# Performance work log

Measured on AMD Instinct MI355X. Metric: run time of the kernel, lower is better.

## Reference

```python
import jax, jax.numpy as jnp
import numpy as np

N, C, H, W = 4, 256, 60, 60
CIMG = 5  # rgb/ir channels after add_position (3 + x + y)
K = 8
ITERS = 2


def setup_inputs() -> dict:
    key = jax.random.key(0)
    ks = jax.random.split(key, 12)
    inp = {
        "cnn_encoder_output": jax.random.normal(ks[0], (N, C, H, W), jnp.float32),
        "rgb": jax.random.normal(ks[1], (N, CIMG, H, W), jnp.float32),
        "ir": jax.random.normal(ks[2], (N, CIMG, H, W), jnp.float32),
        # g-MLP (mlp_num_layers=1): Linear(2C -> C), torch weight layout [out, in]
        "W_g_rgb": jax.random.normal(ks[3], (C, 2 * C), jnp.float32) * 0.02,
        "b_g_rgb": jnp.zeros((C,), jnp.float32),
        "W_g_ir": jax.random.normal(ks[4], (C, 2 * C), jnp.float32) * 0.02,
        "b_g_ir": jnp.zeros((C,), jnp.float32),
        # SE block: Linear(2C -> C//16) -> ReLU -> Linear(C//16 -> C) -> Sigmoid
        "W_se1": jax.random.normal(ks[5], (C // 16, 2 * C), jnp.float32) * 0.02,
        "b_se1": jnp.zeros((C // 16,), jnp.float32),
        "W_se2": jax.random.normal(ks[6], (C, C // 16), jnp.float32) * 0.02,
        "b_se2": jnp.zeros((C,), jnp.float32),
        "gamma": jnp.ones((1,), jnp.float32),
        "gnn_iterations": ITERS,
        "k": K,
    }
    return inp


def _knn_indices(x, k):
    # x: [N, HW, D] -> indices of k nearest neighbours [N, HW, k]
    r = jnp.einsum("nid,njd->nij", x, x)          # gram matrix
    sq = jnp.einsum("nid,nid->ni", x, x)          # squared norms
    d2 = sq[:, :, None] + sq[:, None, :] - 2.0 * r
    d = jnp.sqrt(jnp.maximum(d2, 0.0))
    d = jax.lax.stop_gradient(d)
    _, idx = jax.lax.top_k(-d, k)                  # smallest distances
    return idx


def _gather(h, idx):
    # h: [N, HW, C], idx: [N, HW, K] -> [N, HW, K, C]
    return jax.vmap(lambda hn, i: hn[i])(h, idx)


def reference(cnn_encoder_output, rgb, ir, W_g_rgb, b_g_rgb, W_g_ir, b_g_ir,
              W_se1, b_se1, W_se2, b_se2, gamma, gnn_iterations, k):
    n, c, hh, ww = cnn_encoder_output.shape
    hw = hh * ww
    rgb_f = rgb.reshape(n, rgb.shape[1], hw).transpose(0, 2, 1)  # [N, HW, 5]
    ir_f = ir.reshape(n, ir.shape[1], hw).transpose(0, 2, 1)
    knn_rgb = _knn_indices(rgb_f, k)  # [N, HW, K]
    knn_ir = _knn_indices(ir_f, k)

    h = cnn_encoder_output.transpose(0, 2, 3, 1).reshape(n, hw, c)  # [N, HW, C]

    for _ in range(gnn_iterations):
        rgb_nb = _gather(h, knn_rgb)  # [N, HW, K, C]
        ir_nb = _gather(h, knn_ir)
        rgb_feat = jnp.concatenate([rgb_nb, rgb_nb - ir_nb], axis=-1)  # [N,HW,K,2C]
        ir_feat = jnp.concatenate([ir_nb, ir_nb - rgb_nb], axis=-1)
        m_rgb = jnp.max(jax.nn.relu(jnp.einsum("nhkf,cf->nhkc", rgb_feat, W_g_rgb) + b_g_rgb), axis=2)
        m_ir = jnp.max(jax.nn.relu(jnp.einsum("nhkf,cf->nhkc", ir_feat, W_g_ir) + b_g_ir), axis=2)
        cc = jnp.concatenate([m_rgb, m_ir], axis=-1).mean(axis=1, keepdims=True)  # [N,1,2C]
        se = jax.nn.sigmoid(jax.nn.relu(cc @ W_se1.T + b_se1) @ W_se2.T + b_se2)  # [N,1,C]
        h = se * h

    h = h.reshape(n, hh, ww, c).transpose(0, 3, 1, 2)
    return jax.nn.relu(gamma * h + cnn_encoder_output)
```

## Files before the change

### kernel.cpp

```cpp
#include <hip/hip_runtime.h>
#include <hip/hip_bf16.h>

#define NB 4
#define CH 256
#define HWT 3600
#define KNN 8
#define ITERS 2
#define POSB 16
#define MPAD 3712

#define SSEG 16
#define SEGJ 225

typedef __attribute__((ext_vector_type(8))) __bf16 bf16x8;
typedef __attribute__((ext_vector_type(4))) float f32x4;

__device__ inline float med3f(float a, float b, float c) {
    return __builtin_amdgcn_fmed3f(a, b, c);
}

__global__ void knn_prep(const float* __restrict__ rgb, const float* __restrict__ ir,
                         float* __restrict__ xpack) {
    int t = blockIdx.x * blockDim.x + threadIdx.x;
    if (t >= 2 * NB * HWT) return;
    int nm = t / HWT, j = t - nm * HWT;
    int mod = nm / NB, n = nm - mod * NB;
    const float* x = (mod == 0 ? rgb : ir) + (size_t)n * 5 * HWT;
    float v[5], q = 0.f;
#pragma unroll
    for (int d = 0; d < 5; ++d) { v[d] = x[d * HWT + j]; q = fmaf(v[d], v[d], q); }
    float* o = xpack + (size_t)t * 8;
#pragma unroll
    for (int d = 0; d < 5; ++d) o[d] = v[d];
    o[5] = q; o[6] = 0.f; o[7] = 0.f;
}

__global__ __launch_bounds__(256) void knn_main(const float* __restrict__ xpack,
                                                unsigned* __restrict__ partial) {
    int seg = blockIdx.x, rb = blockIdx.y, nm = blockIdx.z;
    int t = threadIdx.x;
    const float* xp = xpack + (size_t)nm * HWT * 8;
    __shared__ float4 xs[SEGJ * 2];
    const float4* src = ((const float4*)xp) + seg * (SEGJ * 2);
    xs[t] = src[t];
    if (t + 256 < SEGJ * 2) xs[t + 256] = src[t + 256];
    __syncthreads();

    int row = rb * SEGJ + t;
    bool active = (t < SEGJ);
    int rr = active ? row : 0;
    float4 a0 = ((const float4*)xp)[rr * 2];
    float4 b0 = ((const float4*)xp)[rr * 2 + 1];
    float xi0 = a0.x, xi1 = a0.y, xi2 = a0.z, xi3 = a0.w, xi4 = b0.x;
    float qi1 = b0.y + 1.0f;

    const float BIG = __uint_as_float(0x7F000000u);
    float best[8];
#pragma unroll
    for (int i = 0; i < 8; ++i) best[i] = BIG;

    const float2* xs2 = (const float2*)xs;
    unsigned jg0 = (unsigned)(seg * SEGJ);
#pragma unroll 5
    for (int jj = 0; jj < SEGJ; ++jj) {
        float4 a = xs[jj * 2];
        float2 b = xs2[jj * 4 + 2];
        float dot = a.x * xi0;
        dot = fmaf(a.y, xi1, dot);
        dot = fmaf(a.z, xi2, dot);
        dot = fmaf(a.w, xi3, dot);
        dot = fmaf(b.x, xi4, dot);
        float d2 = fmaf(-2.0f, dot, b.y + qi1);
        unsigned kb = (__float_as_uint(d2) & 0xFFFFF000u) | (jg0 + jj);
        float kf = __uint_as_float(kb);
        best[7] = med3f(best[6], best[7], kf);
        best[6] = med3f(best[5], best[6], kf);
        best[5] = med3f(best[4], best[5], kf);
        best[4] = med3f(best[3], best[4], kf);
        best[3] = med3f(best[2], best[3], kf);
        best[2] = med3f(best[1], best[2], kf);
        best[1] = med3f(best[0], best[1], kf);
        best[0] = fminf(best[0], kf);
    }
    if (active) {
        unsigned* o = partial + (((size_t)nm * SSEG + seg) * HWT + row) * 8;
        uint4 lo = { __float_as_uint(best[0]), __float_as_uint(best[1]),
                     __float_as_uint(best[2]), __float_as_uint(best[3]) };
        uint4 hi = { __float_as_uint(best[4]), __float_as_uint(best[5]),
                     __float_as_uint(best[6]), __float_as_uint(best[7]) };
        ((uint4*)o)[0] = lo;
        ((uint4*)o)[1] = hi;
    }
}

__global__ __launch_bounds__(256) void knn_merge(const unsigned* __restrict__ partial,
                                                 int* __restrict__ knn_rgb,
                                                 int* __restrict__ knn_ir) {
    int tid = blockIdx.x * blockDim.x + threadIdx.x;
    if (tid >= 2 * 2 * NB * HWT) return;
    int rid = tid >> 1, sub = tid & 1;
    int nm = rid / HWT, row = rid - nm * HWT;
    const float BIG = __uint_as_float(0x7F000000u);
    float best[8];
#pragma unroll
    for (int i = 0; i < 8; ++i) best[i] = BIG;
    for (int s = sub; s < SSEG; s += 2) {
        const unsigned* p = partial + (((size_t)nm * SSEG + s) * HWT + row) * 8;
#pragma unroll
        for (int w = 0; w < 2; ++w) {
            uint4 v = ((const uint4*)p)[w];
            unsigned vv[4] = { v.x, v.y, v.z, v.w };
#pragma unroll
            for (int e = 0; e < 4; ++e) {
                float kf = __uint_as_float(vv[e]);
                best[7] = med3f(best[6], best[7], kf);
                best[6] = med3f(best[5], best[6], kf);
                best[5] = med3f(best[4], best[5], kf);
                best[4] = med3f(best[3], best[4], kf);
                best[3] = med3f(best[2], best[3], kf);
                best[2] = med3f(best[1], best[2], kf);
                best[1] = med3f(best[0], best[1], kf);
                best[0] = fminf(best[0], kf);
            }
        }
    }
    float other[8];
#pragma unroll
    for (int i = 0; i < 8; ++i) other[i] = __shfl_xor(best[i], 1);
#pragma unroll
    for (int i = 0; i < 8; ++i) {
        float kf = other[i];
        best[7] = med3f(best[6], best[7], kf);
        best[6] = med3f(best[5], best[6], kf);
        best[5] = med3f(best[4], best[5], kf);
        best[4] = med3f(best[3], best[4], kf);
        best[3] = med3f(best[2], best[3], kf);
        best[2] = med3f(best[1], best[2], kf);
        best[1] = med3f(best[0], best[1], kf);
        best[0] = fminf(best[0], kf);
    }
    if (sub == 0) {
        int mod = nm / NB, n = nm - mod * NB;
        int* o = (mod == 0 ? knn_rgb : knn_ir) + ((size_t)n * HWT + row) * KNN;
#pragma unroll
        for (int i = 0; i < 8; ++i) o[i] = (int)(__float_as_uint(best[i]) & 0xFFFu);
    }
}

__global__ void init_kernel(const float* __restrict__ Wg_rgb, const float* __restrict__ Wg_ir,
                            float* __restrict__ Wcomb, float* __restrict__ g) {
    int t = blockIdx.x * blockDim.x + threadIdx.x;
    if (t < 1024 * 256) {
        int o = t >> 8, j = t & 255;
        float v;
        if (o < 256)      v = Wg_rgb[o * 512 + j] + Wg_rgb[o * 512 + 256 + j];
        else if (o < 512) v = Wg_rgb[(o - 256) * 512 + 256 + j];
        else if (o < 768) v = Wg_ir[(o - 512) * 512 + j] + Wg_ir[(o - 512) * 512 + 256 + j];
        else              v = Wg_ir[(o - 768) * 512 + 256 + j];
        Wcomb[t] = v;
    }
    if (t < NB * CH) g[t] = 1.0f;
}

__global__ __launch_bounds__(256) void scale_w(const float* __restrict__ Wcomb,
                                               const float* __restrict__ g,
                                               __hip_bfloat16* __restrict__ Wbf) {
    int n = blockIdx.y;
    int gid = blockIdx.x * 256 + threadIdx.x;
    int o = gid >> 5;
    int kb = (gid & 31) * 8;
    const float* w = Wcomb + o * 256 + kb;
    const float* gp = g + n * CH + kb;
    union { uint4 u; __hip_bfloat16 h[8]; } pk;
#pragma unroll
    for (int i = 0; i < 8; ++i) pk.h[i] = __float2bfloat16(w[i] * gp[i]);
    *(uint4*)(Wbf + ((size_t)n * 1024 + o) * CH + kb) = pk.u;
}

__global__ __launch_bounds__(256) void convert_a(const float* __restrict__ cnn,
                                                 __hip_bfloat16* __restrict__ Abf) {
    __shared__ float st[64][65];
    int n = blockIdx.z, k0 = blockIdx.y * 64, m0 = blockIdx.x * 64;
    int t = threadIdx.x;
    const float* src = cnn + (size_t)n * CH * HWT;
#pragma unroll
    for (int r = 0; r < 4; ++r) {
        int kl = r * 16 + (t >> 4);
        int ms = (t & 15) * 4;
        float4 v = {0.f, 0.f, 0.f, 0.f};
        if (m0 + ms < HWT) v = *(const float4*)(src + (size_t)(k0 + kl) * HWT + m0 + ms);
        st[ms + 0][kl] = v.x; st[ms + 1][kl] = v.y;
        st[ms + 2][kl] = v.z; st[ms + 3][kl] = v.w;
    }
    __syncthreads();
    int m = t >> 2, kg = (t & 3) * 16;
    union { uint4 u[2]; __hip_bfloat16 h[16]; } pk;
#pragma unroll
    for (int i = 0; i < 16; ++i) pk.h[i] = __float2bfloat16(st[m][kg + i]);
    __hip_bfloat16* dst = Abf + ((size_t)n * MPAD + m0 + m) * CH + k0 + kg;
    ((uint4*)dst)[0] = pk.u[0];
    ((uint4*)dst)[1] = pk.u[1];
}

__global__ __launch_bounds__(256) void gemm_mfma(const __hip_bfloat16* __restrict__ Abf,
                                                 const __hip_bfloat16* __restrict__ Wbf,
                                                 __hip_bfloat16* __restrict__ Yall) {
    __shared__ char smem[32768];
    char* sA = smem;
    char* sB = smem + 16384;
    int lid = blockIdx.x;
    int n = blockIdx.y;
    int w = (lid & 7) * 29 + (lid >> 3);
    int m0 = (w >> 3) * 128;
    int o0 = (w & 7) * 128;
    int t = threadIdx.x;
    int lane = t & 63, wid = t >> 6;
    int wm = wid >> 1, wo = wid & 1;

    const __hip_bfloat16* Ab = Abf + (size_t)n * MPAD * CH;
    const __hip_bfloat16* Wb = Wbf + (size_t)n * 1024 * CH;

    f32x4 acc[4][4] = {};

    int srow = t >> 3;
    int sslot = t & 7;
    int swz = (sslot ^ (srow & 7)) << 4;
    int fr = lane & 15;
    int kg = lane >> 4;
    int p = lane & 7;

    uint4 av[4], bv[4];
    auto load_tile = [&](int ks) {
#pragma unroll
        for (int r = 0; r < 4; ++r) {
            int row = srow + 32 * r;
            av[r] = *(const uint4*)(Ab + ((size_t)(m0 + row)) * CH + ks * 64 + sslot * 8);
            bv[r] = *(const uint4*)(Wb + ((size_t)(o0 + row)) * CH + ks * 64 + sslot * 8);
        }
    };
    load_tile(0);

    for (int ks = 0; ks < 4; ++ks) {
        __syncthreads();
#pragma unroll
        for (int r = 0; r < 4; ++r) {
            int row = srow + 32 * r;
            *(uint4*)(sA + row * 128 + swz) = av[r];
            *(uint4*)(sB + row * 128 + swz) = bv[r];
        }
        __syncthreads();
        if (ks < 3) load_tile(ks + 1);
#pragma unroll
        for (int kk = 0; kk < 2; ++kk) {
            bf16x8 hf[4], wf[4];
            int slot = kk * 4 + kg;
            int inrow = (slot ^ p) << 4;
#pragma unroll
            for (int f = 0; f < 4; ++f) {
                hf[f] = *(const bf16x8*)(sA + (wm * 64 + f * 16 + fr) * 128 + inrow);
                wf[f] = *(const bf16x8*)(sB + (wo * 64 + f * 16 + fr) * 128 + inrow);
            }
#pragma unroll
            for (int fa = 0; fa < 4; ++fa)
#pragma unroll
                for (int fb = 0; fb < 4; ++fb)
                    acc[fa][fb] = __builtin_amdgcn_mfma_f32_16x16x32_bf16(
                        wf[fa], hf[fb], acc[fa][fb], 0, 0, 0);
        }
    }

    __syncthreads();
#pragma unroll
    for (int fa = 0; fa < 4; ++fa)
#pragma unroll
        for (int fb = 0; fb < 4; ++fb) {
            int ml = wm * 64 + fb * 16 + fr;
            int ob = (wo * 64 + fa * 16 + kg * 4) * 2;
            f32x4 v = acc[fa][fb];
            union { ushort4 u; __hip_bfloat16 h[4]; } pk;
            pk.h[0] = __float2bfloat16(v.x);
            pk.h[1] = __float2bfloat16(v.y);
            pk.h[2] = __float2bfloat16(v.z);
            pk.h[3] = __float2bfloat16(v.w);
            int swzb = (ob & ~15) ^ ((ml & 15) << 4);
            *(ushort4*)(smem + ml * 256 + swzb + (ob & 15)) = pk.u;
        }
    __syncthreads();
    __hip_bfloat16* Y = Yall + (size_t)n * HWT * 1024;
    int colb = (t & 15) * 16;
#pragma unroll
    for (int i = 0; i < 8; ++i) {
        int row = i * 16 + (t >> 4);
        int grow = m0 + row;
        if (grow < HWT) {
            uint4 v = *(const uint4*)(smem + row * 256 + (colb ^ ((row & 15) << 4)));
            *(uint4*)((char*)Y + (size_t)grow * 2048 + o0 * 2 + colb) = v;
        }
    }
}

__global__ void zero_cc(float* __restrict__ ccsum) {
    int t = blockIdx.x * blockDim.x + threadIdx.x;
    if (t < NB * 512) ccsum[t] = 0.f;
}

__global__ __launch_bounds__(256) void gather_kernel(const __hip_bfloat16* __restrict__ Yall,
                                                     const int* __restrict__ knn_rgb,
                                                     const int* __restrict__ knn_ir,
                                                     const float* __restrict__ b_rgb,
                                                     const float* __restrict__ b_ir,
                                                     float* __restrict__ ccsum) {
    int lid = blockIdx.x;
    int xcd = lid & 7, sub = lid >> 3;
    int wg = (xcd < 4 ? xcd * 113 : 4 * 113 + (xcd - 4) * 112) + sub;
    int n = wg / 225;
    int hwbase = (wg - n * 225) * POSB;
    int t = threadIdx.x;
    int half = t >> 7;
    int cp = (t & 127) << 1;
    __shared__ int sidx[POSB][2][KNN];
    {
        int p = t >> 4, rem = t & 15;
        int hw = hwbase + p;
        int v;
        if (rem < 8) v = knn_rgb[((size_t)n * HWT + hw) * KNN + rem];
        else         v = knn_ir[((size_t)n * HWT + hw) * KNN + (rem - 8)];
        sidx[p][rem >> 3][rem & 7] = v;
    }
    __syncthreads();
    const float* bias = half ? b_ir : b_rgb;
    float b0 = bias[cp], b1 = bias[cp + 1];
    float acc0 = 0.f, acc1 = 0.f;
    const __hip_bfloat16* Y = Yall + (size_t)n * HWT * 1024;
    int offA = half * 512 + cp;
    int offB = half * 512 + 256 + cp;
    for (int p = 0; p < POSB; ++p) {
        float m0 = 0.f, m1 = 0.f;
#pragma unroll
        for (int k = 0; k < KNN; ++k) {
            int jA = sidx[p][half][k];
            int jB = sidx[p][half ^ 1][k];
            unsigned u1 = *(const unsigned*)(Y + (size_t)jA * 1024 + offA);
            unsigned u2 = *(const unsigned*)(Y + (size_t)jB * 1024 + offB);
            float a0 = __uint_as_float(u1 << 16);
            float a1 = __uint_as_float(u1 & 0xFFFF0000u);
            float c0 = __uint_as_float(u2 << 16);
            float c1 = __uint_as_float(u2 & 0xFFFF0000u);
            m0 = fmaxf(m0, a0 - c0 + b0);
            m1 = fmaxf(m1, a1 - c1 + b1);
        }
        acc0 += m0;
        acc1 += m1;
    }
    atomicAdd(&ccsum[n * 512 + half * 256 + cp], acc0);
    atomicAdd(&ccsum[n * 512 + half * 256 + cp + 1], acc1);
}

__global__ __launch_bounds__(256) void se_kernel(const float* __restrict__ ccsum,
                                                 const float* __restrict__ W1,
                                                 const float* __restrict__ b1,
                                                 const float* __restrict__ W2,
                                                 const float* __restrict__ b2,
                                                 float* __restrict__ g) {
    int n = blockIdx.x;
    int t = threadIdx.x;
    __shared__ float hid[16];
    __shared__ float cc[512];
    cc[t] = ccsum[n * 512 + t] * (1.0f / HWT);
    cc[256 + t] = ccsum[n * 512 + 256 + t] * (1.0f / HWT);
    __syncthreads();
    if (t < 16) {
        float s = b1[t];
        for (int j = 0; j < 512; ++j) s = fmaf(W1[t * 512 + j], cc[j], s);
        hid[t] = fmaxf(s, 0.f);
    }
    __syncthreads();
    float s = b2[t];
#pragma unroll
    for (int q = 0; q < 16; ++q) s = fmaf(W2[t * 16 + q], hid[q], s);
    float se = 1.0f / (1.0f + expf(-s));
    g[n * CH + t] *= se;
}

__global__ void final_kernel(const float* __restrict__ cnn, const float* __restrict__ g,
                             const float* __restrict__ gamma, float* __restrict__ out) {
    int t = blockIdx.x * blockDim.x + threadIdx.x;
    if (t >= NB * CH * HWT / 4) return;
    int nc = (t * 4) / HWT;
    float4 x = ((const float4*)cnn)[t];
    float s = gamma[0] * g[nc] + 1.0f;
    float4 o;
    o.x = fmaxf(s * x.x, 0.f);
    o.y = fmaxf(s * x.y, 0.f);
    o.z = fmaxf(s * x.z, 0.f);
    o.w = fmaxf(s * x.w, 0.f);
    ((float4*)out)[t] = o;
}

extern "C" void kernel_launch(void* const* d_in, const int* in_sizes, int n_in,
                              void* d_out, int out_size, void* d_ws, size_t ws_size,
                              hipStream_t stream) {
    const float* cnn    = (const float*)d_in[0];
    const float* rgb    = (const float*)d_in[1];
    const float* ir     = (const float*)d_in[2];
    const float* Wg_rgb = (const float*)d_in[3];
    const float* bg_rgb = (const float*)d_in[4];
    const float* Wg_ir  = (const float*)d_in[5];
    const float* bg_ir  = (const float*)d_in[6];
    const float* Wse1   = (const float*)d_in[7];
    const float* bse1   = (const float*)d_in[8];
    const float* Wse2   = (const float*)d_in[9];
    const float* bse2   = (const float*)d_in[10];
    const float* gamma  = (const float*)d_in[11];
    float* out = (float*)d_out;

    char* ws = (char*)d_ws;
    size_t off = 0;
    float* xpack = (float*)(ws + off); off += (size_t)2 * NB * HWT * 8 * 4;
    int* knn_rgb = (int*)(ws + off); off += (size_t)NB * HWT * KNN * 4;
    int* knn_ir  = (int*)(ws + off); off += (size_t)NB * HWT * KNN * 4;
    float* Wcomb = (float*)(ws + off); off += (size_t)1024 * 256 * 4;
    __hip_bfloat16* Wbf = (__hip_bfloat16*)(ws + off); off += (size_t)NB * 1024 * CH * 2;
    __hip_bfloat16* Abf = (__hip_bfloat16*)(ws + off); off += (size_t)NB * MPAD * CH * 2;
    __hip_bfloat16* Yall = (__hip_bfloat16*)(ws + off);
    unsigned* partial = (unsigned*)Yall;
    off += (size_t)NB * HWT * 1024 * 2;
    float* ccsum = (float*)(ws + off); off += (size_t)NB * 512 * 4;
    float* g     = (float*)(ws + off); off += (size_t)NB * CH * 4;

    knn_prep<<<(2 * NB * HWT + 255) / 256, 256, 0, stream>>>(rgb, ir, xpack);
    knn_main<<<dim3(SSEG, 16, 2 * NB), 256, 0, stream>>>(xpack, partial);
    knn_merge<<<(4 * NB * HWT + 255) / 256, 256, 0, stream>>>(partial, knn_rgb, knn_ir);
    init_kernel<<<1024, 256, 0, stream>>>(Wg_rgb, Wg_ir, Wcomb, g);
    convert_a<<<dim3(MPAD / 64, 4, NB), 256, 0, stream>>>(cnn, Abf);

    for (int it = 0; it < ITERS; ++it) {
        scale_w<<<dim3(128, NB), 256, 0, stream>>>(Wcomb, g, Wbf);
        gemm_mfma<<<dim3(232, NB), 256, 0, stream>>>(Abf, Wbf, Yall);
        zero_cc<<<8, 256, 0, stream>>>(ccsum);
        gather_kernel<<<NB * HWT / POSB, 256, 0, stream>>>(Yall, knn_rgb, knn_ir,
                                                           bg_rgb, bg_ir, ccsum);
        se_kernel<<<NB, 256, 0, stream>>>(ccsum, Wse1, bse1, Wse2, bse2, g);
    }
    final_kernel<<<(NB * CH * HWT / 4 + 255) / 256, 256, 0, stream>>>(cnn, g, gamma, out);
}
```

Measured before the change: 240.7 us.

## Fuse setup kernels and co-schedule first GEMM with KNN search

The independent setup kernels (A conversion, weight combining, KNN prep) are merged into one launch. The first-iteration GEMM runs in the same launch as the KNN distance search, with blocks interleaved so MFMA work and VALU work share the GPU. The first scale_w is skipped because g starts at one, and the zeroing of ccsum is folded into neighbouring kernels, which cuts the launch count. The KNN partial buffer now gets its own workspace instead of aliasing Yall, and segments change to 8 of 450 columns. This costs more workspace, and a single block now runs either GEMM or KNN, so the shared-memory and register budget is set by the heavier of the two.

```diff
diff --git a/kernel.cpp b/kernel.cpp
--- a/kernel.cpp
+++ b/kernel.cpp
@@ -5,12 +5,16 @@
 #define CH 256
 #define HWT 3600
 #define KNN 8
-#define ITERS 2
 #define POSB 16
 #define MPAD 3712
 
-#define SSEG 16
-#define SEGJ 225
+#define SSEGP 8
+#define SEGC 450
+#define ROWB 225
+
+#define GEMM_BLKS 928
+#define KNN_BLKS 1024
+#define B_BLKS 1952
 
 typedef __attribute__((ext_vector_type(8))) __bf16 bf16x8;
 typedef __attribute__((ext_vector_type(4))) float f32x4;
@@ -19,38 +23,128 @@
     return __builtin_amdgcn_fmed3f(a, b, c);
 }
 
-__global__ void knn_prep(const float* __restrict__ rgb, const float* __restrict__ ir,
-                         float* __restrict__ xpack) {
-    int t = blockIdx.x * blockDim.x + threadIdx.x;
-    if (t >= 2 * NB * HWT) return;
-    int nm = t / HWT, j = t - nm * HWT;
-    int mod = nm / NB, n = nm - mod * NB;
-    const float* x = (mod == 0 ? rgb : ir) + (size_t)n * 5 * HWT;
-    float v[5], q = 0.f;
-#pragma unroll
-    for (int d = 0; d < 5; ++d) { v[d] = x[d * HWT + j]; q = fmaf(v[d], v[d], q); }
-    float* o = xpack + (size_t)t * 8;
-#pragma unroll
-    for (int d = 0; d < 5; ++d) o[d] = v[d];
-    o[5] = q; o[6] = 0.f; o[7] = 0.f;
-}
-
-__global__ __launch_bounds__(256) void knn_main(const float* __restrict__ xpack,
-                                                unsigned* __restrict__ partial) {
-    int seg = blockIdx.x, rb = blockIdx.y, nm = blockIdx.z;
+
+__device__ __forceinline__ void gemm_body(int lid, int n,
+                                          const __hip_bfloat16* __restrict__ Abf,
+                                          const __hip_bfloat16* __restrict__ Wbf,
+                                          __hip_bfloat16* __restrict__ Yall,
+                                          char* smem) {
+    char* sA = smem;
+    char* sB = smem + 16384;
+    int w = (lid & 7) * 29 + (lid >> 3);
+    int m0 = (w >> 3) * 128;
+    int o0 = (w & 7) * 128;
+    int t = threadIdx.x;
+    int lane = t & 63, wid = t >> 6;
+    int wm = wid >> 1, wo = wid & 1;
+
+    const __hip_bfloat16* Ab = Abf + (size_t)n * MPAD * CH;
+    const __hip_bfloat16* Wb = Wbf + (size_t)n * 1024 * CH;
+
+    f32x4 acc[4][4] = {};
+
+    int srow = t >> 3;
+    int sslot = t & 7;
+    int swz = (sslot ^ (srow & 7)) << 4;
+    int fr = lane & 15;
+    int kg = lane >> 4;
+    int p = lane & 7;
+
+    uint4 av[4], bv[4];
+    auto load_tile = [&](int ks) {
+#pragma unroll
+        for (int r = 0; r < 4; ++r) {
+            int row = srow + 32 * r;
+            av[r] = *(const uint4*)(Ab + ((size_t)(m0 + row)) * CH + ks * 64 + sslot * 8);
+            bv[r] = *(const uint4*)(Wb + ((size_t)(o0 + row)) * CH + ks * 64 + sslot * 8);
+        }
+    };
+    load_tile(0);
+
+    for (int ks = 0; ks < 4; ++ks) {
+        __syncthreads();
+#pragma unroll
+        for (int r = 0; r < 4; ++r) {
+            int row = srow + 32 * r;
+            *(uint4*)(sA + row * 128 + swz) = av[r];
+            *(uint4*)(sB + row * 128 + swz) = bv[r];
+        }
+        __syncthreads();
+        if (ks < 3) load_tile(ks + 1);
+#pragma unroll
+        for (int kk = 0; kk < 2; ++kk) {
+            bf16x8 hf[4], wf[4];
+            int slot = kk * 4 + kg;
+            int inrow = (slot ^ p) << 4;
+#pragma unroll
+            for (int f = 0; f < 4; ++f) {
+                hf[f] = *(const bf16x8*)(sA + (wm * 64 + f * 16 + fr) * 128 + inrow);
+                wf[f] = *(const bf16x8*)(sB + (wo * 64 + f * 16 + fr) * 128 + inrow);
+            }
+#pragma unroll
+            for (int fa = 0; fa < 4; ++fa)
+#pragma unroll
+                for (int fb = 0; fb < 4; ++fb)
+                    acc[fa][fb] = __builtin_amdgcn_mfma_f32_16x16x32_bf16(
+                        wf[fa], hf[fb], acc[fa][fb], 0, 0, 0);
+        }
+    }
+
+    __syncthreads();
+#pragma unroll
+    for (int fa = 0; fa < 4; ++fa)
+#pragma unroll
+        for (int fb = 0; fb < 4; ++fb) {
+            int ml = wm * 64 + fb * 16 + fr;
+            int ob = (wo * 64 + fa * 16 + kg * 4) * 2;
+            f32x4 v = acc[fa][fb];
+            union { ushort4 u; __hip_bfloat16 h[4]; } pk;
+            pk.h[0] = __float2bfloat16(v.x);
+            pk.h[1] = __float2bfloat16(v.y);
+            pk.h[2] = __float2bfloat16(v.z);
+            pk.h[3] = __float2bfloat16(v.w);
+            int swzb = (ob & ~15) ^ ((ml & 15) << 4);
+            *(ushort4*)(smem + ml * 256 + swzb + (ob & 15)) = pk.u;
+        }
+    __syncthreads();
+    __hip_bfloat16* Y = Yall + (size_t)n * HWT * 1024;
+    int colb = (t & 15) * 16;
+#pragma unroll
+    for (int i = 0; i < 8; ++i) {
+        int row = i * 16 + (t >> 4);
+        int grow = m0 + row;
+        if (grow < HWT) {
+            uint4 v = *(const uint4*)(smem + row * 256 + (colb ^ ((row & 15) << 4)));
+            *(uint4*)((char*)Y + (size_t)grow * 2048 + o0 * 2 + colb) = v;
+        }
+    }
+}
+
+__device__ __forceinline__ void knn_body(int kid, const float* __restrict__ xpack,
+                                         unsigned* __restrict__ partial, char* smem) {
+    int seg = kid & 7;
+    int rb = (kid >> 3) & 15;
+    int nm = kid >> 7;
     int t = threadIdx.x;
     const float* xp = xpack + (size_t)nm * HWT * 8;
-    __shared__ float4 xs[SEGJ * 2];
-    const float4* src = ((const float4*)xp) + seg * (SEGJ * 2);
-    xs[t] = src[t];
-    if (t + 256 < SEGJ * 2) xs[t + 256] = src[t + 256];
-    __syncthreads();
-
-    int row = rb * SEGJ + t;
-    bool active = (t < SEGJ);
+    float4* xs4 = (float4*)smem;
+    float2* xs2 = (float2*)(smem + SEGC * 16);
+    int j0 = seg * SEGC;
+    for (int i = t; i < SEGC; i += 256) {
+        const float4* s = (const float4*)(xp + (size_t)(j0 + i) * 8);
+        float4 a = s[0];
+        float4 b = s[1];
+        xs4[i] = a;
+        float2 tmp; tmp.x = b.x; tmp.y = b.y;
+        xs2[i] = tmp;
+    }
+    __syncthreads();
+
+    int row = rb * ROWB + t;
+    bool active = (t < ROWB);
     int rr = active ? row : 0;
-    float4 a0 = ((const float4*)xp)[rr * 2];
-    float4 b0 = ((const float4*)xp)[rr * 2 + 1];
+    float4 a0 = ((const float4*)xp)[(size_t)rr * 2];
+    float4 b0 = ((const float4*)xp)[(size_t)rr * 2 + 1];
     float xi0 = a0.x, xi1 = a0.y, xi2 = a0.z, xi3 = a0.w, xi4 = b0.x;
     float qi1 = b0.y + 1.0f;
 
@@ -59,12 +153,11 @@
 #pragma unroll
     for (int i = 0; i < 8; ++i) best[i] = BIG;
 
-    const float2* xs2 = (const float2*)xs;
-    unsigned jg0 = (unsigned)(seg * SEGJ);
+    unsigned jg0 = (unsigned)j0;
 #pragma unroll 5
-    for (int jj = 0; jj < SEGJ; ++jj) {
-        float4 a = xs[jj * 2];
-        float2 b = xs2[jj * 4 + 2];
+    for (int jj = 0; jj < SEGC; ++jj) {
+        float4 a = xs4[jj];
+        float2 b = xs2[jj];
         float dot = a.x * xi0;
         dot = fmaf(a.y, xi1, dot);
         dot = fmaf(a.z, xi2, dot);
@@ -83,7 +176,7 @@
         best[0] = fminf(best[0], kf);
     }
     if (active) {
-        unsigned* o = partial + (((size_t)nm * SSEG + seg) * HWT + row) * 8;
+        unsigned* o = partial + (((size_t)(nm * SSEGP + seg)) * HWT + row) * 8;
         uint4 lo = { __float_as_uint(best[0]), __float_as_uint(best[1]),
                      __float_as_uint(best[2]), __float_as_uint(best[3]) };
         uint4 hi = { __float_as_uint(best[4]), __float_as_uint(best[5]),
@@ -93,19 +186,108 @@
     }
 }
 
-__global__ __launch_bounds__(256) void knn_merge(const unsigned* __restrict__ partial,
-                                                 int* __restrict__ knn_rgb,
-                                                 int* __restrict__ knn_ir) {
-    int tid = blockIdx.x * blockDim.x + threadIdx.x;
-    if (tid >= 2 * 2 * NB * HWT) return;
+
+__global__ __launch_bounds__(256) void fusedA(const float* __restrict__ cnn,
+                                              __hip_bfloat16* __restrict__ Abf,
+                                              const float* __restrict__ Wg_rgb,
+                                              const float* __restrict__ Wg_ir,
+                                              float* __restrict__ Wcomb,
+                                              float* __restrict__ g,
+                                              __hip_bfloat16* __restrict__ Wbf,
+                                              const float* __restrict__ rgb,
+                                              const float* __restrict__ ir,
+                                              float* __restrict__ xpack) {
+    int bid = blockIdx.x;
+    int t = threadIdx.x;
+    if (bid < GEMM_BLKS) {
+        __shared__ float st[64][65];
+        int n = bid / 232;
+        int rem = bid - n * 232;
+        int k0 = (rem / 58) * 64;
+        int m0 = (rem % 58) * 64;
+        const float* src = cnn + (size_t)n * CH * HWT;
+#pragma unroll
+        for (int r = 0; r < 4; ++r) {
+            int kl = r * 16 + (t >> 4);
+            int ms = (t & 15) * 4;
+            float4 v = {0.f, 0.f, 0.f, 0.f};
+            if (m0 + ms < HWT) v = *(const float4*)(src + (size_t)(k0 + kl) * HWT + m0 + ms);
+            st[ms + 0][kl] = v.x; st[ms + 1][kl] = v.y;
+            st[ms + 2][kl] = v.z; st[ms + 3][kl] = v.w;
+        }
+        __syncthreads();
+        int m = t >> 2, kg = (t & 3) * 16;
+        union { uint4 u[2]; __hip_bfloat16 h[16]; } pk;
+#pragma unroll
+        for (int i = 0; i < 16; ++i) pk.h[i] = __float2bfloat16(st[m][kg + i]);
+        __hip_bfloat16* dst = Abf + ((size_t)n * MPAD + m0 + m) * CH + k0 + kg;
+        ((uint4*)dst)[0] = pk.u[0];
+        ((uint4*)dst)[1] = pk.u[1];
+    } else if (bid < GEMM_BLKS + 1024) {
+        int e = (bid - GEMM_BLKS) * 256 + t;
+        int o = e >> 8, j = e & 255;
+        float v;
+        if (o < 256)      v = Wg_rgb[o * 512 + j] + Wg_rgb[o * 512 + 256 + j];
+        else if (o < 512) v = Wg_rgb[(o - 256) * 512 + 256 + j];
+        else if (o < 768) v = Wg_ir[(o - 512) * 512 + j] + Wg_ir[(o - 512) * 512 + 256 + j];
+        else              v = Wg_ir[(o - 768) * 512 + 256 + j];
+        Wcomb[e] = v;
+        __hip_bfloat16 h = __float2bfloat16(v);
+#pragma unroll
+        for (int n = 0; n < NB; ++n) Wbf[(size_t)n * 262144 + e] = h;
+        if (e < NB * CH) g[e] = 1.0f;
+    } else {
+        int e = (bid - GEMM_BLKS - 1024) * 256 + t;
+        if (e < 2 * NB * HWT) {
+            int nm = e / HWT, j = e - nm * HWT;
+            int mod = nm / NB, n = nm - mod * NB;
+            const float* x = (mod == 0 ? rgb : ir) + (size_t)n * 5 * HWT;
+            float v[5], q = 0.f;
+#pragma unroll
+            for (int d = 0; d < 5; ++d) { v[d] = x[d * HWT + j]; q = fmaf(v[d], v[d], q); }
+            float* o = xpack + (size_t)e * 8;
+#pragma unroll
+            for (int d = 0; d < 5; ++d) o[d] = v[d];
+            o[5] = q; o[6] = 0.f; o[7] = 0.f;
+        }
+    }
+}
+
+__global__ __launch_bounds__(256) void fusedB(const __hip_bfloat16* __restrict__ Abf,
+                                              const __hip_bfloat16* __restrict__ Wbf,
+                                              __hip_bfloat16* __restrict__ Yall,
+                                              const float* __restrict__ xpack,
+                                              unsigned* __restrict__ partial) {
+    __shared__ char smem[32768];
+    int bid = blockIdx.x;
+    if (((bid & 1) == 0) && bid < 2 * GEMM_BLKS) {
+        int gid = bid >> 1;
+        gemm_body(gid % 232, gid / 232, Abf, Wbf, Yall, smem);
+    } else {
+        int kid = (bid < 2 * GEMM_BLKS) ? (bid >> 1) : (GEMM_BLKS + bid - 2 * GEMM_BLKS);
+        knn_body(kid, xpack, partial, smem);
+    }
+}
+
+__global__ __launch_bounds__(256) void knn_merge_zero(const unsigned* __restrict__ partial,
+                                                      int* __restrict__ knn_rgb,
+                                                      int* __restrict__ knn_ir,
+                                                      float* __restrict__ ccsum) {
+    int bid = blockIdx.x;
+    if (bid >= 450) {
+        int e = (bid - 450) * 256 + threadIdx.x;
+        if (e < NB * 512) ccsum[e] = 0.f;
+        return;
+    }
+    int tid = bid * 256 + threadIdx.x;
     int rid = tid >> 1, sub = tid & 1;
     int nm = rid / HWT, row = rid - nm * HWT;
     const float BIG = __uint_as_float(0x7F000000u);
     float best[8];
 #pragma unroll
     for (int i = 0; i < 8; ++i) best[i] = BIG;
-    for (int s = sub; s < SSEG; s += 2) {
-        const unsigned* p = partial + (((size_t)nm * SSEG + s) * HWT + row) * 8;
+    for (int s = sub; s < SSEGP; s += 2) {
+        const unsigned* p = partial + (((size_t)(nm * SSEGP + s)) * HWT + row) * 8;
 #pragma unroll
         for (int w = 0; w < 2; ++w) {
             uint4 v = ((const uint4*)p)[w];
@@ -147,26 +329,18 @@
     }
 }
 
-__global__ void init_kernel(const float* __restrict__ Wg_rgb, const float* __restrict__ Wg_ir,
-                            float* __restrict__ Wcomb, float* __restrict__ g) {
-    int t = blockIdx.x * blockDim.x + threadIdx.x;
-    if (t < 1024 * 256) {
-        int o = t >> 8, j = t & 255;
-        float v;
-        if (o < 256)      v = Wg_rgb[o * 512 + j] + Wg_rgb[o * 512 + 256 + j];
-        else if (o < 512) v = Wg_rgb[(o - 256) * 512 + 256 + j];
-        else if (o < 768) v = Wg_ir[(o - 512) * 512 + j] + Wg_ir[(o - 512) * 512 + 256 + j];
-        else              v = Wg_ir[(o - 768) * 512 + 256 + j];
-        Wcomb[t] = v;
-    }
-    if (t < NB * CH) g[t] = 1.0f;
-}
-
-__global__ __launch_bounds__(256) void scale_w(const float* __restrict__ Wcomb,
-                                               const float* __restrict__ g,
-                                               __hip_bfloat16* __restrict__ Wbf) {
-    int n = blockIdx.y;
-    int gid = blockIdx.x * 256 + threadIdx.x;
+__global__ __launch_bounds__(256) void scale_w_zero(const float* __restrict__ Wcomb,
+                                                    const float* __restrict__ g,
+                                                    __hip_bfloat16* __restrict__ Wbf,
+                                                    float* __restrict__ ccsum) {
+    int bid = blockIdx.x;
+    if (bid >= 512) {
+        int e = (bid - 512) * 256 + threadIdx.x;
+        if (e < NB * 512) ccsum[e] = 0.f;
+        return;
+    }
+    int n = bid >> 7;
+    int gid = (bid & 127) * 256 + threadIdx.x;
     int o = gid >> 5;
     int kb = (gid & 31) * 8;
     const float* w = Wcomb + o * 256 + kb;
@@ -177,132 +351,14 @@
     *(uint4*)(Wbf + ((size_t)n * 1024 + o) * CH + kb) = pk.u;
 }
 
-__global__ __launch_bounds__(256) void convert_a(const float* __restrict__ cnn,
-                                                 __hip_bfloat16* __restrict__ Abf) {
-    __shared__ float st[64][65];
-    int n = blockIdx.z, k0 = blockIdx.y * 64, m0 = blockIdx.x * 64;
-    int t = threadIdx.x;
-    const float* src = cnn + (size_t)n * CH * HWT;
-#pragma unroll
-    for (int r = 0; r < 4; ++r) {
-        int kl = r * 16 + (t >> 4);
-        int ms = (t & 15) * 4;
-        float4 v = {0.f, 0.f, 0.f, 0.f};
-        if (m0 + ms < HWT) v = *(const float4*)(src + (size_t)(k0 + kl) * HWT + m0 + ms);
-        st[ms + 0][kl] = v.x; st[ms + 1][kl] = v.y;
-        st[ms + 2][kl] = v.z; st[ms + 3][kl] = v.w;
-    }
-    __syncthreads();
-    int m = t >> 2, kg = (t & 3) * 16;
-    union { uint4 u[2]; __hip_bfloat16 h[16]; } pk;
-#pragma unroll
-    for (int i = 0; i < 16; ++i) pk.h[i] = __float2bfloat16(st[m][kg + i]);
-    __hip_bfloat16* dst = Abf + ((size_t)n * MPAD + m0 + m) * CH + k0 + kg;
-    ((uint4*)dst)[0] = pk.u[0];
-    ((uint4*)dst)[1] = pk.u[1];
-}
-
-__global__ __launch_bounds__(256) void gemm_mfma(const __hip_bfloat16* __restrict__ Abf,
-                                                 const __hip_bfloat16* __restrict__ Wbf,
-                                                 __hip_bfloat16* __restrict__ Yall) {
+__global__ __launch_bounds__(256) void gemm_k(const __hip_bfloat16* __restrict__ Abf,
+                                              const __hip_bfloat16* __restrict__ Wbf,
+                                              __hip_bfloat16* __restrict__ Yall) {
     __shared__ char smem[32768];
-    char* sA = smem;
-    char* sB = smem + 16384;
-    int lid = blockIdx.x;
-    int n = blockIdx.y;
-    int w = (lid & 7) * 29 + (lid >> 3);
-    int m0 = (w >> 3) * 128;
-    int o0 = (w & 7) * 128;
-    int t = threadIdx.x;
-    int lane = t & 63, wid = t >> 6;
-    int wm = wid >> 1, wo = wid & 1;
-
-    const __hip_bfloat16* Ab = Abf + (size_t)n * MPAD * CH;
-    const __hip_bfloat16* Wb = Wbf + (size_t)n * 1024 * CH;
-
-    f32x4 acc[4][4] = {};
-
-    int srow = t >> 3;
-    int sslot = t & 7;
-    int swz = (sslot ^ (srow & 7)) << 4;
-    int fr = lane & 15;
-    int kg = lane >> 4;
-    int p = lane & 7;
-
-    uint4 av[4], bv[4];
-    auto load_tile = [&](int ks) {
-#pragma unroll
-        for (int r = 0; r < 4; ++r) {
-            int row = srow + 32 * r;
-            av[r] = *(const uint4*)(Ab + ((size_t)(m0 + row)) * CH + ks * 64 + sslot * 8);
-            bv[r] = *(const uint4*)(Wb + ((size_t)(o0 + row)) * CH + ks * 64 + sslot * 8);
-        }
-    };
-    load_tile(0);
-
-    for (int ks = 0; ks < 4; ++ks) {
-        __syncthreads();
-#pragma unroll
-        for (int r = 0; r < 4; ++r) {
-            int row = srow + 32 * r;
-            *(uint4*)(sA + row * 128 + swz) = av[r];
-            *(uint4*)(sB + row * 128 + swz) = bv[r];
-        }
-        __syncthreads();
-        if (ks < 3) load_tile(ks + 1);
-#pragma unroll
-        for (int kk = 0; kk < 2; ++kk) {
-            bf16x8 hf[4], wf[4];
-            int slot = kk * 4 + kg;
-            int inrow = (slot ^ p) << 4;
-#pragma unroll
-            for (int f = 0; f < 4; ++f) {
-                hf[f] = *(const bf16x8*)(sA + (wm * 64 + f * 16 + fr) * 128 + inrow);
-                wf[f] = *(const bf16x8*)(sB + (wo * 64 + f * 16 + fr) * 128 + inrow);
-            }
-#pragma unroll
-            for (int fa = 0; fa < 4; ++fa)
-#pragma unroll
-                for (int fb = 0; fb < 4; ++fb)
-                    acc[fa][fb] = __builtin_amdgcn_mfma_f32_16x16x32_bf16(
-                        wf[fa], hf[fb], acc[fa][fb], 0, 0, 0);
-        }
-    }
-
-    __syncthreads();
-#pragma unroll
-    for (int fa = 0; fa < 4; ++fa)
-#pragma unroll
-        for (int fb = 0; fb < 4; ++fb) {
-            int ml = wm * 64 + fb * 16 + fr;
-            int ob = (wo * 64 + fa * 16 + kg * 4) * 2;
-            f32x4 v = acc[fa][fb];
-            union { ushort4 u; __hip_bfloat16 h[4]; } pk;
-            pk.h[0] = __float2bfloat16(v.x);
-            pk.h[1] = __float2bfloat16(v.y);
-            pk.h[2] = __float2bfloat16(v.z);
-            pk.h[3] = __float2bfloat16(v.w);
-            int swzb = (ob & ~15) ^ ((ml & 15) << 4);
-            *(ushort4*)(smem + ml * 256 + swzb + (ob & 15)) = pk.u;
-        }
-    __syncthreads();
-    __hip_bfloat16* Y = Yall + (size_t)n * HWT * 1024;
-    int colb = (t & 15) * 16;
-#pragma unroll
-    for (int i = 0; i < 8; ++i) {
-        int row = i * 16 + (t >> 4);
-        int grow = m0 + row;
-        if (grow < HWT) {
-            uint4 v = *(const uint4*)(smem + row * 256 + (colb ^ ((row & 15) << 4)));
-            *(uint4*)((char*)Y + (size_t)grow * 2048 + o0 * 2 + colb) = v;
-        }
-    }
-}
-
-__global__ void zero_cc(float* __restrict__ ccsum) {
-    int t = blockIdx.x * blockDim.x + threadIdx.x;
-    if (t < NB * 512) ccsum[t] = 0.f;
-}
+    int gid = blockIdx.x;
+    gemm_body(gid % 232, gid / 232, Abf, Wbf, Yall, smem);
+}
+
 
 __global__ __launch_bounds__(256) void gather_kernel(const __hip_bfloat16* __restrict__ Yall,
                                                      const int* __restrict__ knn_rgb,
@@ -422,25 +478,21 @@
     float* Wcomb = (float*)(ws + off); off += (size_t)1024 * 256 * 4;
     __hip_bfloat16* Wbf = (__hip_bfloat16*)(ws + off); off += (size_t)NB * 1024 * CH * 2;
     __hip_bfloat16* Abf = (__hip_bfloat16*)(ws + off); off += (size_t)NB * MPAD * CH * 2;
-    __hip_bfloat16* Yall = (__hip_bfloat16*)(ws + off);
-    unsigned* partial = (unsigned*)Yall;
-    off += (size_t)NB * HWT * 1024 * 2;
+    __hip_bfloat16* Yall = (__hip_bfloat16*)(ws + off); off += (size_t)NB * HWT * 1024 * 2;
+    unsigned* partial = (unsigned*)(ws + off);
+    off += (size_t)2 * NB * SSEGP * HWT * 8 * 4;
     float* ccsum = (float*)(ws + off); off += (size_t)NB * 512 * 4;
     float* g     = (float*)(ws + off); off += (size_t)NB * CH * 4;
 
-    knn_prep<<<(2 * NB * HWT + 255) / 256, 256, 0, stream>>>(rgb, ir, xpack);
-    knn_main<<<dim3(SSEG, 16, 2 * NB), 256, 0, stream>>>(xpack, partial);
-    knn_merge<<<(4 * NB * HWT + 255) / 256, 256, 0, stream>>>(partial, knn_rgb, knn_ir);
-    init_kernel<<<1024, 256, 0, stream>>>(Wg_rgb, Wg_ir, Wcomb, g);
-    convert_a<<<dim3(MPAD / 64, 4, NB), 256, 0, stream>>>(cnn, Abf);
-
-    for (int it = 0; it < ITERS; ++it) {
-        scale_w<<<dim3(128, NB), 256, 0, stream>>>(Wcomb, g, Wbf);
-        gemm_mfma<<<dim3(232, NB), 256, 0, stream>>>(Abf, Wbf, Yall);
-        zero_cc<<<8, 256, 0, stream>>>(ccsum);
-        gather_kernel<<<NB * HWT / POSB, 256, 0, stream>>>(Yall, knn_rgb, knn_ir,
-                                                           bg_rgb, bg_ir, ccsum);
-        se_kernel<<<NB, 256, 0, stream>>>(ccsum, Wse1, bse1, Wse2, bse2, g);
-    }
-    final_kernel<<<(NB * CH * HWT / 4 + 255) / 256, 256, 0, stream>>>(cnn, g, gamma, out);
-}
+    fusedA<<<GEMM_BLKS + 1024 + 113, 256, 0, stream>>>(cnn, Abf, Wg_rgb, Wg_ir, Wcomb, g,
+                                                       Wbf, rgb, ir, xpack);
+    fusedB<<<B_BLKS, 256, 0, stream>>>(Abf, Wbf, Yall, xpack, partial);
+    knn_merge_zero<<<458, 256, 0, stream>>>(partial, knn_rgb, knn_ir, ccsum);
+    gather_kernel<<<900, 256, 0, stream>>>(Yall, knn_rgb, knn_ir, bg_rgb, bg_ir, ccsum);
+    se_kernel<<<NB, 256, 0, stream>>>(ccsum, Wse1, bse1, Wse2, bse2, g);
+    scale_w_zero<<<520, 256, 0, stream>>>(Wcomb, g, Wbf, ccsum);
+    gemm_k<<<GEMM_BLKS, 256, 0, stream>>>(Abf, Wbf, Yall);
+    gather_kernel<<<900, 256, 0, stream>>>(Yall, knn_rgb, knn_ir, bg_rgb, bg_ir, ccsum);
+    se_kernel<<<NB, 256, 0, stream>>>(ccsum, Wse1, bse1, Wse2, bse2, g);
+    final_kernel<<<3600, 256, 0, stream>>>(cnn, g, gamma, out);
+}
```

New measurement: 231.1 us. 4.0% less time.
